# Performance work log

Hardware: AMD Instinct MI355X
Metric: run time of the kernel (lower is better)

The kernel has to match this reference:

```python
import jax, jax.numpy as jnp
import numpy as np

N = 50000      # nodes
E = 800000     # edges (before self-loops)
F_IN = 128
H = 4          # heads
C = 64         # per-head channels
G = 64         # graphs in batch
NEG_SLOPE = 0.2


def setup_inputs() -> dict:
    key = jax.random.key(0)
    ks = jax.random.split(key, 20)
    rn = lambda k, shape, s=0.1: (jax.random.normal(k, shape, jnp.float32) * s)
    x = jax.random.normal(ks[0], (N, F_IN), jnp.float32)
    edge_index = jax.random.randint(ks[1], (2, E), 0, N, dtype=jnp.int32)
    batch = jnp.sort(jax.random.randint(ks[2], (N,), 0, G, dtype=jnp.int32))
    return {
        "x": x, "edge_index": edge_index, "batch": batch,
        # layer 0: 128 -> (4 heads x 64), concat
        "W0": rn(ks[3], (F_IN, H * C)), "a_src0": rn(ks[4], (H, C)), "a_dst0": rn(ks[5], (H, C)), "b0": jnp.zeros((H * C,), jnp.float32),
        "W1": rn(ks[6], (H * C, H * C)), "a_src1": rn(ks[7], (H, C)), "a_dst1": rn(ks[8], (H, C)), "b1": jnp.zeros((H * C,), jnp.float32),
        "W2": rn(ks[9], (H * C, C)), "a_src2": rn(ks[10], (1, C)), "a_dst2": rn(ks[11], (1, C)), "b2": jnp.zeros((C,), jnp.float32),
        "lin_w": rn(ks[12], (C, 1)), "lin_b": jnp.zeros((1,), jnp.float32),
    }


def gat_layer(h_in, src, dst, W, a_src, a_dst, b, heads, ch, concat):
    n = h_in.shape[0]
    h = (h_in @ W).reshape(n, heads, ch)                         # [N,H,C]
    e_src = jnp.sum(h * a_src[None], axis=-1)                    # [N,H]
    e_dst = jnp.sum(h * a_dst[None], axis=-1)                    # [N,H]
    e = jax.nn.leaky_relu(e_src[src] + e_dst[dst], NEG_SLOPE)    # [E,H]
    # segment softmax over incoming edges of each destination node
    m = jax.ops.segment_max(e, dst, num_segments=n)
    m = jnp.where(jnp.isneginf(m), 0.0, m)
    ex = jnp.exp(e - m[dst])
    denom = jax.ops.segment_sum(ex, dst, num_segments=n)
    alpha = ex / (denom[dst] + 1e-16)                            # [E,H]
    out = jax.ops.segment_sum(h[src] * alpha[:, :, None], dst, num_segments=n)  # [N,H,C]
    out = out.reshape(n, heads * ch) if concat else out.mean(axis=1)
    return out + b


def reference(x, edge_index, batch, W0, a_src0, a_dst0, b0, W1, a_src1, a_dst1, b1, W2, a_src2, a_dst2, b2, lin_w, lin_b):
    n = x.shape[0]
    loops = jnp.arange(n, dtype=edge_index.dtype)
    src = jnp.concatenate([edge_index[0], loops])  # PyG add_self_loops=True
    dst = jnp.concatenate([edge_index[1], loops])
    h = jax.nn.relu(gat_layer(x, src, dst, W0, a_src0, a_dst0, b0, H, C, True))
    h = jax.nn.relu(gat_layer(h, src, dst, W1, a_src1, a_dst1, b1, H, C, True))
    h = gat_layer(h, src, dst, W2, a_src2, a_dst2, b2, 1, C, False)  # [N,64]
    # global mean pool per graph
    counts = jax.ops.segment_sum(jnp.ones((n,), h.dtype), batch, num_segments=G)
    pooled = jax.ops.segment_sum(h, batch, num_segments=G) / jnp.maximum(counts, 1.0)[:, None]
    return pooled @ lin_w + lin_b  # [G,1]
```

## Files before the change

### kernel.cpp

```cpp
#include <hip/hip_runtime.h>
#include <math.h>

typedef __bf16 bf16x8 __attribute__((ext_vector_type(8)));
typedef __bf16 bf16x4 __attribute__((ext_vector_type(4)));
typedef float f32x4 __attribute__((ext_vector_type(4)));
typedef float f32x2 __attribute__((ext_vector_type(2)));
typedef unsigned int u32x2 __attribute__((ext_vector_type(2)));
typedef unsigned int u32x4 __attribute__((ext_vector_type(4)));

#define LOG2E 1.4426950408889634f
#define BCAP 8192

static __device__ __forceinline__ float lrelu(float e) { return fmaxf(e, 0.2f * e); }
static __device__ __forceinline__ float fexp2(float x) { return __builtin_amdgcn_exp2f(x); }

static __device__ __forceinline__ int cmap(int p) {
  return (p & ~63) + (p & 3) * 16 + ((p & 63) >> 2);
}

__global__ void prep_kernel(const float* __restrict__ W0, __bf16* __restrict__ Bt0,
                            const float* __restrict__ W1, __bf16* __restrict__ Bt1,
                            const float* __restrict__ W2, __bf16* __restrict__ Bt2, int FIN,
                            int* __restrict__ cnt, int n) {
  int b = blockIdx.x;
  if (b < 256) {
    for (int k = threadIdx.x; k < FIN; k += 256) Bt0[b * FIN + k] = (__bf16)W0[k * 256 + b];
    return;
  }
  b -= 256;
  if (b < 256) {
    int k = threadIdx.x;
    Bt1[b * 256 + k] = (__bf16)W1[cmap(k) * 256 + b];
    return;
  }
  b -= 256;
  if (b < 64) {
    int k = threadIdx.x;
    Bt2[b * 256 + k] = (__bf16)W2[cmap(k) * 64 + b];
    return;
  }
  b -= 64;
  int i = b * 256 + threadIdx.x;
  if (i < n) cnt[i] = 0;
}

template <int K, int NT>
__global__ __launch_bounds__(256) void gemm_part_kernel(
    const float* __restrict__ A, const __bf16* __restrict__ Bt,
    const float* __restrict__ a_src, const float* __restrict__ a_dst,
    unsigned char* __restrict__ C, float* __restrict__ es, float* __restrict__ ed, int M,
    int gmx, const int* __restrict__ srcE, const int* __restrict__ dstE,
    int* __restrict__ bucket_cnt, unsigned int* __restrict__ part, int E, int EE, int n) {
  constexpr int Nc = NT * 64;
  constexpr int H = NT;
  constexpr int KS = K / 32;
  __shared__ __bf16 Bs[2][NT * 64][40];
  if ((int)blockIdx.x >= gmx) {
    int tid = threadIdx.x;
    int* hist = (int*)&Bs[0][0][0];
    int* gbase = hist + 256;
    hist[tid] = 0;
    __syncthreads();
    int ab = ((int)blockIdx.x - gmx) * 4096;
    int sv[16], dv[16];
#pragma unroll
    for (int t = 0; t < 16; t++) {
      int e = ab + t * 256 + tid;
      if (e < EE) {
        if (e < E) { sv[t] = srcE[e]; dv[t] = dstE[e]; }
        else { sv[t] = dv[t] = e - E; }
      } else { sv[t] = -1; dv[t] = 0; }
    }
    int lr[16];
#pragma unroll
    for (int t = 0; t < 16; t++)
      if (sv[t] >= 0) lr[t] = atomicAdd(&hist[dv[t] >> 8], 1);
    __syncthreads();
    int NB = (n + 255) >> 8;
    gbase[tid] = (tid < NB && hist[tid] > 0) ? atomicAdd(&bucket_cnt[tid * 16], hist[tid]) : 0;
    __syncthreads();
#pragma unroll
    for (int t = 0; t < 16; t++)
      if (sv[t] >= 0) {
        int bk = dv[t] >> 8;
        part[(size_t)bk * BCAP + gbase[bk] + lr[t]] =
            (unsigned int)sv[t] | ((unsigned int)(dv[t] & 255) << 24);
      }
    return;
  }
  int bid = blockIdx.x;
  int tid = threadIdx.x;
  int wave = tid >> 6;
  int lane = tid & 63;
  int quad = lane >> 4;
  int l16 = lane & 15;
  int rowBase = bid * 64 + wave * 16;
  f32x4 acc[NT * 4] = {};
  int arow = rowBase + l16;
  arow = (arow < M) ? arow : (M - 1);
  const float* Aptr = &A[(size_t)arow * K + quad * 8];
  int sr = tid >> 2;
  int sc = (tid & 3) * 8;
  bf16x8 af[KS];
#pragma unroll
  for (int s = 0; s < KS; s++) {
    f32x4 lo = *(const f32x4*)&Aptr[s * 32];
    f32x4 hi = *(const f32x4*)&Aptr[s * 32 + 4];
    bf16x8 t;
    t[0] = (__bf16)lo.x; t[1] = (__bf16)lo.y; t[2] = (__bf16)lo.z; t[3] = (__bf16)lo.w;
    t[4] = (__bf16)hi.x; t[5] = (__bf16)hi.y; t[6] = (__bf16)hi.z; t[7] = (__bf16)hi.w;
    af[s] = t;
  }
#pragma unroll
  for (int it = 0; it < NT; it++) {
    int r = it * 64 + sr;
    *(bf16x8*)&Bs[0][r][sc] = *(const bf16x8*)&Bt[(size_t)r * K + sc];
  }
  __syncthreads();
#pragma unroll
  for (int s = 0; s < KS; s++) {
    int cur = s & 1;
    if (s + 1 < KS) {
#pragma unroll
      for (int it = 0; it < NT; it++) {
        int r = it * 64 + sr;
        *(bf16x8*)&Bs[cur ^ 1][r][sc] = *(const bf16x8*)&Bt[(size_t)r * K + (s + 1) * 32 + sc];
      }
    }
#pragma unroll
    for (int ng = 0; ng < NT * 4; ng++) {
      bf16x8 b = *(const bf16x8*)&Bs[cur][ng * 16 + l16][quad * 8];
      acc[ng] = __builtin_amdgcn_mfma_f32_16x16x32_bf16(af[s], b, acc[ng], 0, 0, 0);
    }
    __syncthreads();
  }
  float asv[NT * 4], adv[NT * 4];
#pragma unroll
  for (int ng = 0; ng < NT * 4; ng++) {
    int c = (ng >> 2) * 64 + (ng & 3) * 16 + l16;
    asv[ng] = a_src[c];
    adv[ng] = a_dst[c];
  }
#pragma unroll
  for (int r = 0; r < 4; r++) {
    int row = rowBase + quad * 4 + r;
#pragma unroll
    for (int h = 0; h < H; h++) {
      float ss = 0.f, sd = 0.f;
#pragma unroll
      for (int g = 0; g < 4; g++) {
        float hv = acc[h * 4 + g][r];
        ss += hv * asv[h * 4 + g];
        sd += hv * adv[h * 4 + g];
      }
#pragma unroll
      for (int o = 1; o < 16; o <<= 1) {
        ss += __shfl_xor(ss, o);
        sd += __shfl_xor(sd, o);
      }
      if (row < M) {
        if (l16 == 0) {
          es[row * H + h] = ss * LOG2E;
          ed[row * H + h] = sd * LOG2E;
        }
        unsigned int pk = 0;
        pk = __builtin_amdgcn_cvt_pk_fp8_f32(acc[h * 4 + 0][r], acc[h * 4 + 1][r], pk, false);
        pk = __builtin_amdgcn_cvt_pk_fp8_f32(acc[h * 4 + 2][r], acc[h * 4 + 3][r], pk, true);
        *(unsigned int*)&C[(size_t)row * Nc + h * 64 + l16 * 4] = pk;
      }
    }
  }
}

__global__ __launch_bounds__(1024) void bucket_csr_kernel(
    const unsigned int* __restrict__ part, const int* __restrict__ bucket_cnt,
    int* __restrict__ offsets, int* __restrict__ src_sorted, int n, int EE) {
  __shared__ int sc[256];
  __shared__ int excl[256];
  __shared__ int run[256];
  int tid = threadIdx.x;
  int b = blockIdx.x;
  int NB = (n + 255) >> 8;
  if (tid < 256) sc[tid] = (tid < NB) ? bucket_cnt[tid * 16] : 0;
  __syncthreads();
  for (int d = 1; d < 256; d <<= 1) {
    int t = 0;
    if (tid < 256 && tid >= d) t = sc[tid - d];
    __syncthreads();
    if (tid < 256) sc[tid] += t;
    __syncthreads();
  }
  int base = (b == 0) ? 0 : sc[b - 1];
  int cb = sc[b] - base;
  const unsigned int* mypart = part + (size_t)b * BCAP;
  if (tid < 256) run[tid] = 0;
  __syncthreads();
  for (int i = tid; i < cb; i += 1024) atomicAdd(&run[mypart[i] >> 24], 1);
  __syncthreads();
  int myc = (tid < 256) ? run[tid] : 0;
  if (tid < 256) sc[tid] = myc;
  __syncthreads();
  for (int d = 1; d < 256; d <<= 1) {
    int t = 0;
    if (tid < 256 && tid >= d) t = sc[tid - d];
    __syncthreads();
    if (tid < 256) sc[tid] += t;
    __syncthreads();
  }
  if (tid < 256) {
    excl[tid] = sc[tid] - myc;
    int node = b * 256 + tid;
    if (node < n) offsets[node] = base + excl[tid];
    run[tid] = 0;
  }
  if (b == 0 && tid == 0) offsets[n] = EE;
  __syncthreads();
  for (int i = tid; i < cb; i += 1024) {
    unsigned int p = mypart[i];
    int j = p >> 24;
    int r = atomicAdd(&run[j], 1);
    src_sorted[base + excl[j] + r] = (int)(p & 0xFFFFFFu);
  }
}

template <int K, int NT>
__global__ __launch_bounds__(256) void gemm2_kernel(const __bf16* __restrict__ A,
                                                    const __bf16* __restrict__ Bt,
                                                    const float* __restrict__ a_src,
                                                    const float* __restrict__ a_dst,
                                                    unsigned char* __restrict__ C,
                                                    float* __restrict__ es,
                                                    float* __restrict__ ed, int M) {
  constexpr int Nc = NT * 64;
  constexpr int H = NT;
  constexpr int KS = K / 32;
  __shared__ __bf16 Bs[2][NT * 64][40];
  int tid = threadIdx.x;
  int wave = tid >> 6;
  int lane = tid & 63;
  int quad = lane >> 4;
  int l16 = lane & 15;
  int rowBase = blockIdx.x * 64 + wave * 16;
  f32x4 acc[NT * 4] = {};
  int arow = rowBase + l16;
  arow = (arow < M) ? arow : (M - 1);
  const __bf16* Aptr = &A[(size_t)arow * K + quad * 8];
  int sr = tid >> 2;
  int sc = (tid & 3) * 8;
  bf16x8 af[KS];
#pragma unroll
  for (int s = 0; s < KS; s++) af[s] = *(const bf16x8*)&Aptr[s * 32];
#pragma unroll
  for (int it = 0; it < NT; it++) {
    int r = it * 64 + sr;
    *(bf16x8*)&Bs[0][r][sc] = *(const bf16x8*)&Bt[(size_t)r * K + sc];
  }
  __syncthreads();
#pragma unroll
  for (int s = 0; s < KS; s++) {
    int cur = s & 1;
    if (s + 1 < KS) {
#pragma unroll
      for (int it = 0; it < NT; it++) {
        int r = it * 64 + sr;
        *(bf16x8*)&Bs[cur ^ 1][r][sc] = *(const bf16x8*)&Bt[(size_t)r * K + (s + 1) * 32 + sc];
      }
    }
#pragma unroll
    for (int ng = 0; ng < NT * 4; ng++) {
      bf16x8 b = *(const bf16x8*)&Bs[cur][ng * 16 + l16][quad * 8];
      acc[ng] = __builtin_amdgcn_mfma_f32_16x16x32_bf16(af[s], b, acc[ng], 0, 0, 0);
    }
    __syncthreads();
  }
  float asv[NT * 4], adv[NT * 4];
#pragma unroll
  for (int ng = 0; ng < NT * 4; ng++) {
    int c = (ng >> 2) * 64 + (ng & 3) * 16 + l16;
    asv[ng] = a_src[c];
    adv[ng] = a_dst[c];
  }
#pragma unroll
  for (int r = 0; r < 4; r++) {
    int row = rowBase + quad * 4 + r;
#pragma unroll
    for (int h = 0; h < H; h++) {
      float ss = 0.f, sd = 0.f;
#pragma unroll
      for (int g = 0; g < 4; g++) {
        float hv = acc[h * 4 + g][r];
        ss += hv * asv[h * 4 + g];
        sd += hv * adv[h * 4 + g];
      }
#pragma unroll
      for (int o = 1; o < 16; o <<= 1) {
        ss += __shfl_xor(ss, o);
        sd += __shfl_xor(sd, o);
      }
      if (row < M) {
        if (l16 == 0) {
          es[row * H + h] = ss * LOG2E;
          ed[row * H + h] = sd * LOG2E;
        }
        unsigned int pk = 0;
        pk = __builtin_amdgcn_cvt_pk_fp8_f32(acc[h * 4 + 0][r], acc[h * 4 + 1][r], pk, false);
        pk = __builtin_amdgcn_cvt_pk_fp8_f32(acc[h * 4 + 2][r], acc[h * 4 + 3][r], pk, true);
        *(unsigned int*)&C[(size_t)row * Nc + h * 64 + l16 * 4] = pk;
      }
    }
  }
}

__global__ void agg256_kernel(const unsigned char* __restrict__ h, const int* __restrict__ offsets,
                              const int* __restrict__ src_sorted, const float* __restrict__ es,
                              const float* __restrict__ ed, const float* __restrict__ bias,
                              __bf16* __restrict__ out, int n) {
  int node = blockIdx.x * (blockDim.x >> 6) + (threadIdx.x >> 6);
  int lane = threadIdx.x & 63;
  if (node >= n) return;
  int quad = lane >> 4;
  int l16 = lane & 15;
  unsigned hd = (unsigned)(l16 >> 2);
  unsigned cOff = (unsigned)(l16 * 16);
  float myEd = ed[node * 4 + hd];
  int off = offsets[node];
  int deg = offsets[node + 1] - off;
  int idxr = (lane < deg) ? src_sorted[off + lane] : 0;
  float acc[16] = {};
  float sw = 0.f;
  int npre = (deg < 64 ? deg : 64) & ~7;
  int j = 0;
  float eA0 = 0.f, eA1 = 0.f;
  u32x4 uA0 = {}, uA1 = {};
  if (j + 8 <= npre) {
    unsigned sA0 = (unsigned)__shfl(idxr, j + quad);
    unsigned sA1 = (unsigned)__shfl(idxr, j + 4 + quad);
    eA0 = es[sA0 * 4u + hd];
    eA1 = es[sA1 * 4u + hd];
    uA0 = *(const u32x4*)(h + (sA0 << 8) + cOff);
    uA1 = *(const u32x4*)(h + (sA1 << 8) + cOff);
  }
  while (j + 8 <= npre) {
    int jn = j + 8;
    float eB0 = 0.f, eB1 = 0.f;
    u32x4 uB0 = {}, uB1 = {};
    if (jn + 8 <= npre) {
      unsigned sB0 = (unsigned)__shfl(idxr, jn + quad);
      unsigned sB1 = (unsigned)__shfl(idxr, jn + 4 + quad);
      eB0 = es[sB0 * 4u + hd];
      eB1 = es[sB1 * 4u + hd];
      uB0 = *(const u32x4*)(h + (sB0 << 8) + cOff);
      uB1 = *(const u32x4*)(h + (sB1 << 8) + cOff);
    }
    float w0 = fexp2(lrelu(eA0 + myEd));
    float w1 = fexp2(lrelu(eA1 + myEd));
    sw += w0 + w1;
#pragma unroll
    for (int i = 0; i < 4; i++) {
      f32x2 a = __builtin_amdgcn_cvt_pk_f32_fp8(uA0[i], false);
      f32x2 b = __builtin_amdgcn_cvt_pk_f32_fp8(uA0[i], true);
      acc[i * 4 + 0] += w0 * a.x;
      acc[i * 4 + 1] += w0 * a.y;
      acc[i * 4 + 2] += w0 * b.x;
      acc[i * 4 + 3] += w0 * b.y;
    }
#pragma unroll
    for (int i = 0; i < 4; i++) {
      f32x2 a = __builtin_amdgcn_cvt_pk_f32_fp8(uA1[i], false);
      f32x2 b = __builtin_amdgcn_cvt_pk_f32_fp8(uA1[i], true);
      acc[i * 4 + 0] += w1 * a.x;
      acc[i * 4 + 1] += w1 * a.y;
      acc[i * 4 + 2] += w1 * b.x;
      acc[i * 4 + 3] += w1 * b.y;
    }
    eA0 = eB0; eA1 = eB1; uA0 = uB0; uA1 = uB1;
    j = jn;
  }
  for (; j < deg; j += 4) {
    if (quad < deg - j) {
      unsigned s = (unsigned)src_sorted[off + j + quad];
      float w = fexp2(lrelu(es[s * 4u + hd] + myEd));
      sw += w;
      u32x4 u = *(const u32x4*)(h + (s << 8) + cOff);
#pragma unroll
      for (int i = 0; i < 4; i++) {
        f32x2 a = __builtin_amdgcn_cvt_pk_f32_fp8(u[i], false);
        f32x2 b = __builtin_amdgcn_cvt_pk_f32_fp8(u[i], true);
        acc[i * 4 + 0] += w * a.x;
        acc[i * 4 + 1] += w * a.y;
        acc[i * 4 + 2] += w * b.x;
        acc[i * 4 + 3] += w * b.y;
      }
    }
  }
  sw += __shfl_xor(sw, 16);
  sw += __shfl_xor(sw, 32);
#pragma unroll
  for (int k = 0; k < 16; k++) {
    acc[k] += __shfl_xor(acc[k], 16);
    acc[k] += __shfl_xor(acc[k], 32);
  }
  float invS = 1.0f / (sw + 1e-16f);
  if (quad == 0) {
    bf16x8 o0, o1;
#pragma unroll
    for (int k = 0; k < 16; k++) {
      int c = (int)hd * 64 + (k & 3) * 16 + (l16 & 3) * 4 + (k >> 2);
      float v = fmaxf(acc[k] * invS + bias[c], 0.f);
      if (k < 8) o0[k] = (__bf16)v; else o1[k - 8] = (__bf16)v;
    }
    *(bf16x8*)&out[(size_t)node * 256 + l16 * 16] = o0;
    *(bf16x8*)&out[(size_t)node * 256 + l16 * 16 + 8] = o1;
  }
}

__global__ void agg64_kernel(const unsigned char* __restrict__ h, const int* __restrict__ offsets,
                             const int* __restrict__ src_sorted, const float* __restrict__ es,
                             const float* __restrict__ ed, const float* __restrict__ bias,
                             const float* __restrict__ lin_w, float* __restrict__ pnode, int n) {
  int node = blockIdx.x * (blockDim.x >> 6) + (threadIdx.x >> 6);
  int lane = threadIdx.x & 63;
  if (node >= n) return;
  int grp = lane >> 3;
  int l8 = lane & 7;
  unsigned cOff = (unsigned)(l8 * 8);
  float myEd = ed[node];
  int off = offsets[node];
  int deg = offsets[node + 1] - off;
  int idxr = (lane < deg) ? src_sorted[off + lane] : 0;
  float acc[8] = {};
  float sw = 0.f;
  int npre = (deg < 64 ? deg : 64) & ~7;
  int j = 0;
  float eA = 0.f;
  u32x2 uA = {};
  if (j + 8 <= npre) {
    unsigned sA = (unsigned)__shfl(idxr, j + grp);
    eA = es[sA];
    uA = *(const u32x2*)(h + (sA << 6) + cOff);
  }
  while (j + 8 <= npre) {
    int jn = j + 8;
    float eB = 0.f;
    u32x2 uB = {};
    if (jn + 8 <= npre) {
      unsigned sB = (unsigned)__shfl(idxr, jn + grp);
      eB = es[sB];
      uB = *(const u32x2*)(h + (sB << 6) + cOff);
    }
    float w = fexp2(lrelu(eA + myEd));
    sw += w;
    {
      f32x2 a = __builtin_amdgcn_cvt_pk_f32_fp8(uA.x, false);
      f32x2 b = __builtin_amdgcn_cvt_pk_f32_fp8(uA.x, true);
      f32x2 c = __builtin_amdgcn_cvt_pk_f32_fp8(uA.y, false);
      f32x2 d = __builtin_amdgcn_cvt_pk_f32_fp8(uA.y, true);
      acc[0] += w * a.x; acc[1] += w * a.y; acc[2] += w * b.x; acc[3] += w * b.y;
      acc[4] += w * c.x; acc[5] += w * c.y; acc[6] += w * d.x; acc[7] += w * d.y;
    }
    eA = eB; uA = uB;
    j = jn;
  }
  for (; j < deg; j += 8) {
    if (grp < deg - j) {
      unsigned s = (unsigned)src_sorted[off + j + grp];
      float w = fexp2(lrelu(es[s] + myEd));
      sw += w;
      u32x2 u = *(const u32x2*)(h + (s << 6) + cOff);
      f32x2 a = __builtin_amdgcn_cvt_pk_f32_fp8(u.x, false);
      f32x2 b = __builtin_amdgcn_cvt_pk_f32_fp8(u.x, true);
      f32x2 c = __builtin_amdgcn_cvt_pk_f32_fp8(u.y, false);
      f32x2 d = __builtin_amdgcn_cvt_pk_f32_fp8(u.y, true);
      acc[0] += w * a.x; acc[1] += w * a.y; acc[2] += w * b.x; acc[3] += w * b.y;
      acc[4] += w * c.x; acc[5] += w * c.y; acc[6] += w * d.x; acc[7] += w * d.y;
    }
  }
#pragma unroll
  for (int o = 8; o < 64; o <<= 1) {
    sw += __shfl_xor(sw, o);
#pragma unroll
    for (int k = 0; k < 8; k++) acc[k] += __shfl_xor(acc[k], o);
  }
  float invS = 1.0f / (sw + 1e-16f);
  float p = 0.f;
#pragma unroll
  for (int k = 0; k < 8; k++) {
    int c = (k & 3) * 16 + l8 * 2 + (k >> 2);
    p += (acc[k] * invS + bias[c]) * lin_w[c];
  }
#pragma unroll
  for (int o = 1; o < 8; o <<= 1) p += __shfl_xor(p, o);
  if (lane == 0) pnode[node] = p;
}

static __device__ __forceinline__ int lowerb(const int* __restrict__ a, int n, int key) {
  int lo = 0, hi = n;
  while (lo < hi) {
    int mid = (lo + hi) >> 1;
    if (a[mid] < key) lo = mid + 1; else hi = mid;
  }
  return lo;
}

__global__ void poolfinal_kernel(const float* __restrict__ pnode, const int* __restrict__ batch,
                                 const float* __restrict__ lin_b, float* __restrict__ out, int n) {
  __shared__ float ws[4];
  int g = blockIdx.x;
  int start = lowerb(batch, n, g);
  int end = lowerb(batch, n, g + 1);
  float acc = 0.f;
  for (int i = start + threadIdx.x; i < end; i += 256) acc += pnode[i];
  for (int o = 32; o > 0; o >>= 1) acc += __shfl_down(acc, o);
  if ((threadIdx.x & 63) == 0) ws[threadIdx.x >> 6] = acc;
  __syncthreads();
  if (threadIdx.x == 0) {
    float total = ws[0] + ws[1] + ws[2] + ws[3];
    out[g] = total / fmaxf((float)(end - start), 1.0f) + lin_b[0];
  }
}

extern "C" void kernel_launch(void* const* d_in, const int* in_sizes, int n_in, void* d_out,
                              int out_size, void* d_ws, size_t ws_size, hipStream_t stream) {
  const float* x = (const float*)d_in[0];
  const int* edge_index = (const int*)d_in[1];
  const int* batch = (const int*)d_in[2];
  const float* W0 = (const float*)d_in[3];
  const float* a_src0 = (const float*)d_in[4];
  const float* a_dst0 = (const float*)d_in[5];
  const float* b0 = (const float*)d_in[6];
  const float* W1 = (const float*)d_in[7];
  const float* a_src1 = (const float*)d_in[8];
  const float* a_dst1 = (const float*)d_in[9];
  const float* b1 = (const float*)d_in[10];
  const float* W2 = (const float*)d_in[11];
  const float* a_src2 = (const float*)d_in[12];
  const float* a_dst2 = (const float*)d_in[13];
  const float* b2 = (const float*)d_in[14];
  const float* lin_w = (const float*)d_in[15];
  const float* lin_b = (const float*)d_in[16];
  float* out = (float*)d_out;

  const int N = in_sizes[2];
  const int E = in_sizes[1] / 2;
  const int EE = E + N;
  const int G = 64;
  const int FIN = in_sizes[0] / N;

  const int* srcArr = edge_index;
  const int* dstArr = edge_index + E;

  size_t off = 0;
  auto alloc = [&](size_t bytes) -> void* {
    off = (off + 255) & ~(size_t)255;
    void* p = (char*)d_ws + off;
    off += bytes;
    return p;
  };
  unsigned char* hA = (unsigned char*)alloc((size_t)N * 256);
  __bf16* hB = (__bf16*)alloc((size_t)N * 256 * 2);
  unsigned char* h2 = (unsigned char*)alloc((size_t)N * 64);
  float* pnode = (float*)alloc((size_t)N * 4);
  __bf16* Bt0 = (__bf16*)alloc((size_t)256 * FIN * 2);
  __bf16* Bt1 = (__bf16*)alloc((size_t)256 * 256 * 2);
  __bf16* Bt2 = (__bf16*)alloc((size_t)64 * 256 * 2);
  float* es = (float*)alloc((size_t)N * 4 * 4);
  float* ed = (float*)alloc((size_t)N * 4 * 4);
  int* offsets = (int*)alloc((size_t)(N + 1) * 4);
  int* src_sorted = (int*)alloc((size_t)EE * 4);
  int* bucket_cnt = (int*)alloc((size_t)4096 * 4);
  (void)ws_size;

  int NB = (N + 255) >> 8;

  unsigned int* part = (unsigned int*)hB;

  int nwb = (N + 3) / 4;
  int gmx = (N + 63) / 64;
  int nA = (EE + 4095) / 4096;

  prep_kernel<<<576 + 16, 256, 0, stream>>>(W0, Bt0, W1, Bt1, W2, Bt2, FIN, bucket_cnt, 4096);

  gemm_part_kernel<128, 4><<<gmx + nA, 256, 0, stream>>>(
      x, Bt0, a_src0, a_dst0, hA, es, ed, N, gmx, srcArr, dstArr, bucket_cnt, part, E, EE, N);

  bucket_csr_kernel<<<NB, 1024, 0, stream>>>(part, bucket_cnt, offsets, src_sorted, N, EE);

  agg256_kernel<<<nwb, 256, 0, stream>>>(hA, offsets, src_sorted, es, ed, b0, hB, N);

  gemm2_kernel<256, 4><<<gmx, 256, 0, stream>>>(hB, Bt1, a_src1, a_dst1, hA, es, ed, N);
  agg256_kernel<<<nwb, 256, 0, stream>>>(hA, offsets, src_sorted, es, ed, b1, hB, N);

  gemm2_kernel<256, 1><<<gmx, 256, 0, stream>>>(hB, Bt2, a_src2, a_dst2, h2, es, ed, N);
  agg64_kernel<<<nwb, 256, 0, stream>>>(h2, offsets, src_sorted, es, ed, b2, lin_w, pnode, N);

  poolfinal_kernel<<<G, 256, 0, stream>>>(pnode, batch, lin_b, out, N);
}
```

Baseline: 277.4 us.

## Fold final GAT layer and linear head into scalar projections per node

Since the final layer has a single head and is followed by a linear projection, W2 is folded into lin_w, a_src2 and a_dst2 to give three 256-vectors. The layer-1 aggregation now emits only a scalar value q plus source and destination attention logits per node, with no full hidden state. The layer-2 GEMM and the 64-channel gathers are replaced by a scalar softmax-weighted sum. This removes a kernel launch, the hB write and reread, and the 64-byte per-edge gathers, at the cost of different rounding (fp32 instead of a bf16/fp8 intermediate).

After: 263.4 us. -5.0%, faster.

```diff
diff --git a/kernel.cpp b/kernel.cpp
--- a/kernel.cpp
+++ b/kernel.cpp
@@ -19,9 +19,12 @@
 }
 
 __global__ void prep_kernel(const float* __restrict__ W0, __bf16* __restrict__ Bt0,
-                            const float* __restrict__ W1, __bf16* __restrict__ Bt1,
-                            const float* __restrict__ W2, __bf16* __restrict__ Bt2, int FIN,
-                            int* __restrict__ cnt, int n) {
+                            const float* __restrict__ W1, __bf16* __restrict__ Bt1, int FIN,
+                            const float* __restrict__ W2, const float* __restrict__ lin_w,
+                            const float* __restrict__ a_src2, const float* __restrict__ a_dst2,
+                            const float* __restrict__ b2, float* __restrict__ wt,
+                            float* __restrict__ vas, float* __restrict__ vad,
+                            float* __restrict__ bc, int* __restrict__ cnt, int n) {
   int b = blockIdx.x;
   if (b < 256) {
     for (int k = threadIdx.x; k < FIN; k += 256) Bt0[b * FIN + k] = (__bf16)W0[k * 256 + b];
@@ -34,12 +37,26 @@
     return;
   }
   b -= 256;
-  if (b < 64) {
-    int k = threadIdx.x;
-    Bt2[b * 256 + k] = (__bf16)W2[cmap(k) * 64 + b];
+  if (b == 0) {
+    int c = threadIdx.x;
+    float qv = 0.f, sv = 0.f, dv = 0.f;
+    for (int k = 0; k < 64; k++) {
+      float wv = W2[c * 64 + k];
+      qv += wv * lin_w[k];
+      sv += wv * a_src2[k];
+      dv += wv * a_dst2[k];
+    }
+    wt[c] = qv;
+    vas[c] = sv;
+    vad[c] = dv;
+    if (c == 0) {
+      float s = 0.f;
+      for (int k = 0; k < 64; k++) s += b2[k] * lin_w[k];
+      bc[0] = s;
+    }
     return;
   }
-  b -= 64;
+  b -= 1;
   int i = b * 256 + threadIdx.x;
   if (i < n) cnt[i] = 0;
 }
@@ -414,83 +431,145 @@
   }
 }
 
-__global__ void agg64_kernel(const unsigned char* __restrict__ h, const int* __restrict__ offsets,
-                             const int* __restrict__ src_sorted, const float* __restrict__ es,
-                             const float* __restrict__ ed, const float* __restrict__ bias,
-                             const float* __restrict__ lin_w, float* __restrict__ pnode, int n) {
+__global__ void agg256f_kernel(const unsigned char* __restrict__ h, const int* __restrict__ offsets,
+                               const int* __restrict__ src_sorted, const float* __restrict__ es,
+                               const float* __restrict__ ed, const float* __restrict__ bias,
+                               const float* __restrict__ wt, const float* __restrict__ vas,
+                               const float* __restrict__ vad, f32x2* __restrict__ qes,
+                               float* __restrict__ ed2, int n) {
   int node = blockIdx.x * (blockDim.x >> 6) + (threadIdx.x >> 6);
   int lane = threadIdx.x & 63;
   if (node >= n) return;
-  int grp = lane >> 3;
-  int l8 = lane & 7;
-  unsigned cOff = (unsigned)(l8 * 8);
-  float myEd = ed[node];
+  int quad = lane >> 4;
+  int l16 = lane & 15;
+  unsigned hd = (unsigned)(l16 >> 2);
+  unsigned cOff = (unsigned)(l16 * 16);
+  float myEd = ed[node * 4 + hd];
   int off = offsets[node];
   int deg = offsets[node + 1] - off;
   int idxr = (lane < deg) ? src_sorted[off + lane] : 0;
-  float acc[8] = {};
+  float acc[16] = {};
   float sw = 0.f;
   int npre = (deg < 64 ? deg : 64) & ~7;
   int j = 0;
-  float eA = 0.f;
-  u32x2 uA = {};
+  float eA0 = 0.f, eA1 = 0.f;
+  u32x4 uA0 = {}, uA1 = {};
   if (j + 8 <= npre) {
-    unsigned sA = (unsigned)__shfl(idxr, j + grp);
-    eA = es[sA];
-    uA = *(const u32x2*)(h + (sA << 6) + cOff);
+    unsigned sA0 = (unsigned)__shfl(idxr, j + quad);
+    unsigned sA1 = (unsigned)__shfl(idxr, j + 4 + quad);
+    eA0 = es[sA0 * 4u + hd];
+    eA1 = es[sA1 * 4u + hd];
+    uA0 = *(const u32x4*)(h + (sA0 << 8) + cOff);
+    uA1 = *(const u32x4*)(h + (sA1 << 8) + cOff);
   }
   while (j + 8 <= npre) {
     int jn = j + 8;
-    float eB = 0.f;
-    u32x2 uB = {};
+    float eB0 = 0.f, eB1 = 0.f;
+    u32x4 uB0 = {}, uB1 = {};
     if (jn + 8 <= npre) {
-      unsigned sB = (unsigned)__shfl(idxr, jn + grp);
-      eB = es[sB];
-      uB = *(const u32x2*)(h + (sB << 6) + cOff);
-    }
-    float w = fexp2(lrelu(eA + myEd));
+      unsigned sB0 = (unsigned)__shfl(idxr, jn + quad);
+      unsigned sB1 = (unsigned)__shfl(idxr, jn + 4 + quad);
+      eB0 = es[sB0 * 4u + hd];
+      eB1 = es[sB1 * 4u + hd];
+      uB0 = *(const u32x4*)(h + (sB0 << 8) + cOff);
+      uB1 = *(const u32x4*)(h + (sB1 << 8) + cOff);
+    }
+    float w0 = fexp2(lrelu(eA0 + myEd));
+    float w1 = fexp2(lrelu(eA1 + myEd));
+    sw += w0 + w1;
+#pragma unroll
+    for (int i = 0; i < 4; i++) {
+      f32x2 a = __builtin_amdgcn_cvt_pk_f32_fp8(uA0[i], false);
+      f32x2 b = __builtin_amdgcn_cvt_pk_f32_fp8(uA0[i], true);
+      acc[i * 4 + 0] += w0 * a.x;
+      acc[i * 4 + 1] += w0 * a.y;
+      acc[i * 4 + 2] += w0 * b.x;
+      acc[i * 4 + 3] += w0 * b.y;
+    }
+#pragma unroll
+    for (int i = 0; i < 4; i++) {
+      f32x2 a = __builtin_amdgcn_cvt_pk_f32_fp8(uA1[i], false);
+      f32x2 b = __builtin_amdgcn_cvt_pk_f32_fp8(uA1[i], true);
+      acc[i * 4 + 0] += w1 * a.x;
+      acc[i * 4 + 1] += w1 * a.y;
+      acc[i * 4 + 2] += w1 * b.x;
+      acc[i * 4 + 3] += w1 * b.y;
+    }
+    eA0 = eB0; eA1 = eB1; uA0 = uB0; uA1 = uB1;
+    j = jn;
+  }
+  for (; j < deg; j += 4) {
+    if (quad < deg - j) {
+      unsigned s = (unsigned)src_sorted[off + j + quad];
+      float w = fexp2(lrelu(es[s * 4u + hd] + myEd));
+      sw += w;
+      u32x4 u = *(const u32x4*)(h + (s << 8) + cOff);
+#pragma unroll
+      for (int i = 0; i < 4; i++) {
+        f32x2 a = __builtin_amdgcn_cvt_pk_f32_fp8(u[i], false);
+        f32x2 b = __builtin_amdgcn_cvt_pk_f32_fp8(u[i], true);
+        acc[i * 4 + 0] += w * a.x;
+        acc[i * 4 + 1] += w * a.y;
+        acc[i * 4 + 2] += w * b.x;
+        acc[i * 4 + 3] += w * b.y;
+      }
+    }
+  }
+  sw += __shfl_xor(sw, 16);
+  sw += __shfl_xor(sw, 32);
+#pragma unroll
+  for (int k = 0; k < 16; k++) {
+    acc[k] += __shfl_xor(acc[k], 16);
+    acc[k] += __shfl_xor(acc[k], 32);
+  }
+  float invS = 1.0f / (sw + 1e-16f);
+  float q = 0.f, s2 = 0.f, d2 = 0.f;
+#pragma unroll
+  for (int k = 0; k < 16; k++) {
+    int c = (int)hd * 64 + (k & 3) * 16 + (l16 & 3) * 4 + (k >> 2);
+    float v = fmaxf(acc[k] * invS + bias[c], 0.f);
+    q += v * wt[c];
+    s2 += v * vas[c];
+    d2 += v * vad[c];
+  }
+#pragma unroll
+  for (int o = 1; o < 16; o <<= 1) {
+    q += __shfl_xor(q, o);
+    s2 += __shfl_xor(s2, o);
+    d2 += __shfl_xor(d2, o);
+  }
+  if (lane == 0) {
+    f32x2 r;
+    r.x = q;
+    r.y = s2 * LOG2E;
+    qes[node] = r;
+    ed2[node] = d2 * LOG2E;
+  }
+}
+
+__global__ void agg64v2_kernel(const f32x2* __restrict__ qes, const float* __restrict__ ed2,
+                               const int* __restrict__ offsets, const int* __restrict__ src_sorted,
+                               const float* __restrict__ bc, float* __restrict__ pnode, int n) {
+  int node = blockIdx.x * (blockDim.x >> 6) + (threadIdx.x >> 6);
+  int lane = threadIdx.x & 63;
+  if (node >= n) return;
+  float myEd = ed2[node];
+  int off = offsets[node];
+  int deg = offsets[node + 1] - off;
+  float sw = 0.f, swq = 0.f;
+  for (int j = lane; j < deg; j += 64) {
+    int s = src_sorted[off + j];
+    f32x2 v = qes[s];
+    float w = fexp2(lrelu(v.y + myEd));
     sw += w;
-    {
-      f32x2 a = __builtin_amdgcn_cvt_pk_f32_fp8(uA.x, false);
-      f32x2 b = __builtin_amdgcn_cvt_pk_f32_fp8(uA.x, true);
-      f32x2 c = __builtin_amdgcn_cvt_pk_f32_fp8(uA.y, false);
-      f32x2 d = __builtin_amdgcn_cvt_pk_f32_fp8(uA.y, true);
-      acc[0] += w * a.x; acc[1] += w * a.y; acc[2] += w * b.x; acc[3] += w * b.y;
-      acc[4] += w * c.x; acc[5] += w * c.y; acc[6] += w * d.x; acc[7] += w * d.y;
-    }
-    eA = eB; uA = uB;
-    j = jn;
-  }
-  for (; j < deg; j += 8) {
-    if (grp < deg - j) {
-      unsigned s = (unsigned)src_sorted[off + j + grp];
-      float w = fexp2(lrelu(es[s] + myEd));
-      sw += w;
-      u32x2 u = *(const u32x2*)(h + (s << 6) + cOff);
-      f32x2 a = __builtin_amdgcn_cvt_pk_f32_fp8(u.x, false);
-      f32x2 b = __builtin_amdgcn_cvt_pk_f32_fp8(u.x, true);
-      f32x2 c = __builtin_amdgcn_cvt_pk_f32_fp8(u.y, false);
-      f32x2 d = __builtin_amdgcn_cvt_pk_f32_fp8(u.y, true);
-      acc[0] += w * a.x; acc[1] += w * a.y; acc[2] += w * b.x; acc[3] += w * b.y;
-      acc[4] += w * c.x; acc[5] += w * c.y; acc[6] += w * d.x; acc[7] += w * d.y;
-    }
-  }
-#pragma unroll
-  for (int o = 8; o < 64; o <<= 1) {
+    swq += w * v.x;
+  }
+#pragma unroll
+  for (int o = 1; o < 64; o <<= 1) {
     sw += __shfl_xor(sw, o);
-#pragma unroll
-    for (int k = 0; k < 8; k++) acc[k] += __shfl_xor(acc[k], o);
-  }
-  float invS = 1.0f / (sw + 1e-16f);
-  float p = 0.f;
-#pragma unroll
-  for (int k = 0; k < 8; k++) {
-    int c = (k & 3) * 16 + l8 * 2 + (k >> 2);
-    p += (acc[k] * invS + bias[c]) * lin_w[c];
-  }
-#pragma unroll
-  for (int o = 1; o < 8; o <<= 1) p += __shfl_xor(p, o);
-  if (lane == 0) pnode[node] = p;
+    swq += __shfl_xor(swq, o);
+  }
+  if (lane == 0) pnode[node] = swq / (sw + 1e-16f) + bc[0];
 }
 
 static __device__ __forceinline__ int lowerb(const int* __restrict__ a, int n, int key) {
@@ -558,16 +637,20 @@
   };
   unsigned char* hA = (unsigned char*)alloc((size_t)N * 256);
   __bf16* hB = (__bf16*)alloc((size_t)N * 256 * 2);
-  unsigned char* h2 = (unsigned char*)alloc((size_t)N * 64);
   float* pnode = (float*)alloc((size_t)N * 4);
   __bf16* Bt0 = (__bf16*)alloc((size_t)256 * FIN * 2);
   __bf16* Bt1 = (__bf16*)alloc((size_t)256 * 256 * 2);
-  __bf16* Bt2 = (__bf16*)alloc((size_t)64 * 256 * 2);
   float* es = (float*)alloc((size_t)N * 4 * 4);
   float* ed = (float*)alloc((size_t)N * 4 * 4);
   int* offsets = (int*)alloc((size_t)(N + 1) * 4);
   int* src_sorted = (int*)alloc((size_t)EE * 4);
   int* bucket_cnt = (int*)alloc((size_t)4096 * 4);
+  f32x2* qes = (f32x2*)alloc((size_t)N * 8);
+  float* ed2 = (float*)alloc((size_t)N * 4);
+  float* wt = (float*)alloc(256 * 4);
+  float* vas = (float*)alloc(256 * 4);
+  float* vad = (float*)alloc(256 * 4);
+  float* bc = (float*)alloc(256);
   (void)ws_size;
 
   int NB = (N + 255) >> 8;
@@ -578,7 +661,9 @@
   int gmx = (N + 63) / 64;
   int nA = (EE + 4095) / 4096;
 
-  prep_kernel<<<576 + 16, 256, 0, stream>>>(W0, Bt0, W1, Bt1, W2, Bt2, FIN, bucket_cnt, 4096);
+  prep_kernel<<<256 + 256 + 1 + 16, 256, 0, stream>>>(W0, Bt0, W1, Bt1, FIN, W2, lin_w, a_src2,
+                                                      a_dst2, b2, wt, vas, vad, bc, bucket_cnt,
+                                                      4096);
 
   gemm_part_kernel<128, 4><<<gmx + nA, 256, 0, stream>>>(
       x, Bt0, a_src0, a_dst0, hA, es, ed, N, gmx, srcArr, dstArr, bucket_cnt, part, E, EE, N);
@@ -588,10 +673,11 @@
   agg256_kernel<<<nwb, 256, 0, stream>>>(hA, offsets, src_sorted, es, ed, b0, hB, N);
 
   gemm2_kernel<256, 4><<<gmx, 256, 0, stream>>>(hB, Bt1, a_src1, a_dst1, hA, es, ed, N);
-  agg256_kernel<<<nwb, 256, 0, stream>>>(hA, offsets, src_sorted, es, ed, b1, hB, N);
-
-  gemm2_kernel<256, 1><<<gmx, 256, 0, stream>>>(hB, Bt2, a_src2, a_dst2, h2, es, ed, N);
-  agg64_kernel<<<nwb, 256, 0, stream>>>(h2, offsets, src_sorted, es, ed, b2, lin_w, pnode, N);
+
+  agg256f_kernel<<<nwb, 256, 0, stream>>>(hA, offsets, src_sorted, es, ed, b1, wt, vas, vad, qes,
+                                          ed2, N);
+
+  agg64v2_kernel<<<nwb, 256, 0, stream>>>(qes, ed2, offsets, src_sorted, bc, pnode, N);
 
   poolfinal_kernel<<<G, 256, 0, stream>>>(pnode, batch, lin_b, out, N);
 }
```
